# Performance work log

Measured on AMD Instinct MI355X. Metric: run time of the kernel, lower is better.

## Reference

```python
import jax, jax.numpy as jnp
import numpy as np

D_MODEL = 1024
H = 16
D_K = D_MODEL // H
B = 4
S = 2048
NEG = -1.0e9


def setup_inputs() -> dict:
    key = jax.random.key(0)
    ks = jax.random.split(key, 12)
    scale = 1.0 / np.sqrt(D_MODEL)
    inp = {
        "q": jax.random.normal(ks[0], (B, S, D_MODEL), jnp.float32),
        "k": jax.random.normal(ks[1], (B, S, D_MODEL), jnp.float32),
        "v": jax.random.normal(ks[2], (B, S, D_MODEL), jnp.float32),
        "mask": jax.random.randint(ks[3], (1, 1, S, S), 0, 2, jnp.int32),
        # nn.Linear params: y = x @ W.T + b
        "Wq": jax.random.normal(ks[4], (D_MODEL, D_MODEL), jnp.float32) * scale,
        "bq": jnp.zeros((D_MODEL,), jnp.float32),
        "Wk": jax.random.normal(ks[5], (D_MODEL, D_MODEL), jnp.float32) * scale,
        "bk": jnp.zeros((D_MODEL,), jnp.float32),
        "Wv": jax.random.normal(ks[6], (D_MODEL, D_MODEL), jnp.float32) * scale,
        "bv": jnp.zeros((D_MODEL,), jnp.float32),
        "Wo": jax.random.normal(ks[7], (D_MODEL, D_MODEL), jnp.float32) * scale,
        "bo": jnp.zeros((D_MODEL,), jnp.float32),
    }
    return inp


def reference(q, k, v, mask, Wq, bq, Wk, bk, Wv, bv, Wo, bo):
    # QKV projections (torch Linear: x @ W.T + b)
    query = q @ Wq.T + bq                       # [B,S,D]
    key_ = k @ Wk.T + bk
    value = v @ Wv.T + bv
    # [B,S,D] -> [B,H,S,d_k]
    def split_heads(x):
        return x.reshape(B, S, H, D_K).transpose(0, 2, 1, 3)
    query, key_, value = split_heads(query), split_heads(key_), split_heads(value)
    # scaled dot-product attention
    scores = jnp.einsum("bhqd,bhkd->bhqk", query, key_) / np.sqrt(D_K)
    scores = jnp.where(mask == 0, NEG, scores)  # masked_fill(mask==0, -1e9)
    attn = jax.nn.softmax(scores, axis=-1)      # dropout p=0 -> identity
    x = jnp.einsum("bhqk,bhkd->bhqd", attn, value)
    # merge heads and output projection
    x = x.transpose(0, 2, 1, 3).reshape(B, S, D_MODEL)
    return x @ Wo.T + bo
```

## Files before the change

### kernel.cpp

```cpp
#include <hip/hip_runtime.h>
#include <hip/hip_bf16.h>

typedef __bf16 bf16;
typedef __bf16 bf16x8 __attribute__((ext_vector_type(8)));
typedef __bf16 bf16x4 __attribute__((ext_vector_type(4)));
typedef float  f32x4v __attribute__((ext_vector_type(4)));

#define MFMA16(a, b, c) __builtin_amdgcn_mfma_f32_16x16x32_bf16((a), (b), (c), 0, 0, 0)

static constexpr int D_MODEL = 1024;
static constexpr int NH      = 16;
static constexpr int DK      = 64;
static constexpr int BATCH   = 4;
static constexpr int SEQ     = 2048;

__device__ __forceinline__ void glds16(const void* g, void* l) {
    __builtin_amdgcn_global_load_lds((const __attribute__((address_space(1))) void*)g,
                                     (__attribute__((address_space(3))) void*)l, 16, 0, 0);
}

struct CvtArgs {
    const float* s[7];
    bf16* d[7];
    int n[7];
};

__global__ __launch_bounds__(256) void cvt7(CvtArgs a) {
    const int which = blockIdx.y;
    const int i = (blockIdx.x * 256 + threadIdx.x) * 8;
    if (i >= a.n[which]) return;
    const float4 v0 = *(const float4*)(a.s[which] + i);
    const float4 v1 = *(const float4*)(a.s[which] + i + 4);
    bf16x8 o = {(bf16)v0.x, (bf16)v0.y, (bf16)v0.z, (bf16)v0.w,
                (bf16)v1.x, (bf16)v1.y, (bf16)v1.z, (bf16)v1.w};
    *(bf16x8*)(a.d[which] + i) = o;
}

__global__ __launch_bounds__(256) void mask_prep(const int* __restrict__ m,
                                                 bf16* __restrict__ Mr) {
    const int o = blockIdx.x * 256 + threadIdx.x;
    const int row = o >> 11, j = o & 2047;
    const int g = j >> 6, idx = j & 63;
    const int incol = (g << 6) + ((idx & 3) << 4) + (idx >> 2);
    Mr[o] = (bf16)(float)m[row * 2048 + incol];
}

template <int MODE>
__global__ __launch_bounds__(256) void gemm_bt(const bf16* __restrict__ A,
                                               const bf16* __restrict__ W,
                                               const float* __restrict__ bias,
                                               void* __restrict__ outv) {
    __shared__ bf16 Als[128 * 32];
    __shared__ bf16 Bls[128 * 32];

    const int tid  = threadIdx.x;
    const int wave = tid >> 6;
    const int lane = tid & 63;
    const int l15  = lane & 15;
    const int quad = lane >> 4;
    const int m0   = blockIdx.y * 128;
    const int n0   = blockIdx.x * 128;
    const int wm   = (wave >> 1) * 64;
    const int wn   = (wave & 1) * 64;

    f32x4v acc[4][4];
#pragma unroll
    for (int i = 0; i < 4; ++i)
#pragma unroll
        for (int j = 0; j < 4; ++j) acc[i][j] = (f32x4v){0.f, 0.f, 0.f, 0.f};

    const int r_a    = wave * 16 + (lane >> 2);
    const int c_a    = (lane & 3) * 8;
    const int ldsoff = wave * 512;

    for (int k0 = 0; k0 < 1024; k0 += 32) {
        __syncthreads();
#pragma unroll
        for (int p = 0; p < 2; ++p) {
            const int row = p * 64 + r_a;
            glds16(A + (size_t)(m0 + row) * 1024 + k0 + c_a, &Als[p * 2048 + ldsoff]);
            glds16(W + (size_t)(n0 + row) * 1024 + k0 + c_a, &Bls[p * 2048 + ldsoff]);
        }
        __syncthreads();

        bf16x8 af[4], bfr[4];
#pragma unroll
        for (int i = 0; i < 4; ++i)
            af[i] = *(const bf16x8*)(&Als[(wm + i * 16 + l15) * 32 + quad * 8]);
#pragma unroll
        for (int j = 0; j < 4; ++j)
            bfr[j] = *(const bf16x8*)(&Bls[(wn + j * 16 + l15) * 32 + quad * 8]);
#pragma unroll
        for (int i = 0; i < 4; ++i)
#pragma unroll
            for (int j = 0; j < 4; ++j) acc[i][j] = MFMA16(af[i], bfr[j], acc[i][j]);
    }

#pragma unroll
    for (int j = 0; j < 4; ++j) {
        const int col = n0 + wn + j * 16 + l15;
        const float bs = bias[col];
        const int h = col >> 6, dk = col & 63;
#pragma unroll
        for (int i = 0; i < 4; ++i) {
            const int r4 = m0 + wm + i * 16 + quad * 4;
            const int b = r4 >> 11, sb = r4 & 2047;
            if (MODE == 2) {
                float* out = (float*)outv;
#pragma unroll
                for (int reg = 0; reg < 4; ++reg)
                    out[(size_t)(r4 + reg) * 1024 + col] = acc[i][j][reg] + bs;
            } else if (MODE == 0) {
                bf16* out = (bf16*)outv;
#pragma unroll
                for (int reg = 0; reg < 4; ++reg)
                    out[((size_t)(b * NH + h) * SEQ + sb + reg) * 64 + dk] =
                        (bf16)(acc[i][j][reg] + bs);
            } else {
                bf16* out = (bf16*)outv;
                bf16x4 v = {(bf16)(acc[i][j][0] + bs), (bf16)(acc[i][j][1] + bs),
                            (bf16)(acc[i][j][2] + bs), (bf16)(acc[i][j][3] + bs)};
                *(bf16x4*)(&out[((size_t)((b * NH + h) * 64 + dk)) * SEQ + sb]) = v;
            }
        }
    }
}

__global__ __launch_bounds__(256) void attn_kernel(const bf16* __restrict__ Qh,
                                                   const bf16* __restrict__ Kh,
                                                   const bf16* __restrict__ Vtg,
                                                   const bf16* __restrict__ Mr,
                                                   bf16* __restrict__ Xout) {
    __shared__ bf16 Kls[4096];
    __shared__ bf16 Vls[4096];
    __shared__ bf16 Pls[256 * 72];

    const int tid  = threadIdx.x;
    const int wave = tid >> 6;
    const int lane = tid & 63;
    const int l15  = lane & 15;
    const int quad = lane >> 4;
    const int bh   = blockIdx.x;
    const int q0   = blockIdx.y * 256;

    const size_t base = (size_t)bh * SEQ * DK;
    const bf16* Q  = Qh + base;
    const bf16* K  = Kh + base;
    const bf16* Vg = Vtg + base;

    const int qw = q0 + wave * 64;
    bf16x8 aq[4][2];
#pragma unroll
    for (int rb = 0; rb < 4; ++rb)
#pragma unroll
        for (int hf = 0; hf < 2; ++hf)
            aq[rb][hf] = *(const bf16x8*)(Q + (size_t)(qw + rb * 16 + l15) * 64 +
                                          hf * 32 + quad * 8);

    f32x4v acc[4][4];
    float lsum[4][4];
#pragma unroll
    for (int rb = 0; rb < 4; ++rb)
#pragma unroll
        for (int x = 0; x < 4; ++x) {
            acc[rb][x] = (f32x4v){0.f, 0.f, 0.f, 0.f};
            lsum[rb][x] = 0.f;
        }

    constexpr float CLOG = 0.125f * 1.4426950408889634f;
    const bf16* mbase = Mr + (size_t)(qw + quad * 4) * 2048 + l15 * 4;

    for (int kt = 0; kt < SEQ; kt += 64) {
        __syncthreads();
#pragma unroll
        for (int p = 0; p < 2; ++p) {
            const int kc = wave * 2 + p;
            glds16(K + (size_t)(kt + lane) * 64 + kc * 8, &Kls[kc * 512]);
            glds16(Vg + (size_t)lane * SEQ + kt + kc * 8, &Vls[kc * 512]);
        }
        bf16x4 mv[4][4];
#pragma unroll
        for (int rb = 0; rb < 4; ++rb)
#pragma unroll
            for (int reg = 0; reg < 4; ++reg)
                mv[rb][reg] = *(const bf16x4*)(mbase + (size_t)(rb * 16 + reg) * 2048 + kt);
        __syncthreads();

        bf16x8 bk[4][2];
#pragma unroll
        for (int n16 = 0; n16 < 4; ++n16)
#pragma unroll
            for (int kk = 0; kk < 2; ++kk)
                bk[n16][kk] = *(const bf16x8*)(&Kls[((kk * 4 + quad) * 64 + n16 * 16 + l15) * 8]);

#pragma unroll
        for (int rb = 0; rb < 4; ++rb) {
            f32x4v sv[4];
#pragma unroll
            for (int n16 = 0; n16 < 4; ++n16) {
                f32x4v t = (f32x4v){0.f, 0.f, 0.f, 0.f};
                t = MFMA16(aq[rb][0], bk[n16][0], t);
                t = MFMA16(aq[rb][1], bk[n16][1], t);
                sv[n16] = t;
            }
            const int prow0 = wave * 64 + rb * 16 + quad * 4;
#pragma unroll
            for (int reg = 0; reg < 4; ++reg) {
#pragma unroll
                for (int n16 = 0; n16 < 4; ++n16) {
                    const float e =
                        exp2f(sv[n16][reg] * CLOG) * (float)mv[rb][reg][n16];
                    lsum[rb][reg] += e;
                    Pls[(prow0 + reg) * 72 + n16 * 16 + l15] = (bf16)e;
                }
            }
        }

        bf16x8 pf[4][2];
#pragma unroll
        for (int rb = 0; rb < 4; ++rb)
#pragma unroll
            for (int kc2 = 0; kc2 < 2; ++kc2)
                pf[rb][kc2] = *(const bf16x8*)(&Pls[(wave * 64 + rb * 16 + l15) * 72 +
                                                    kc2 * 32 + quad * 8]);
#pragma unroll
        for (int nt = 0; nt < 4; ++nt) {
            const bf16x8 bv0 = *(const bf16x8*)(&Vls[(quad * 64 + nt * 16 + l15) * 8]);
            const bf16x8 bv1 = *(const bf16x8*)(&Vls[((4 + quad) * 64 + nt * 16 + l15) * 8]);
#pragma unroll
            for (int rb = 0; rb < 4; ++rb) {
                acc[rb][nt] = MFMA16(pf[rb][0], bv0, acc[rb][nt]);
                acc[rb][nt] = MFMA16(pf[rb][1], bv1, acc[rb][nt]);
            }
        }
    }

    const int b = bh >> 4, h = bh & 15;
#pragma unroll
    for (int rb = 0; rb < 4; ++rb) {
        float rinv[4];
#pragma unroll
        for (int reg = 0; reg < 4; ++reg) {
            float l = lsum[rb][reg];
            l += __shfl_xor(l, 1, 16);
            l += __shfl_xor(l, 2, 16);
            l += __shfl_xor(l, 4, 16);
            l += __shfl_xor(l, 8, 16);
            rinv[reg] = 1.0f / l;
        }
#pragma unroll
        for (int nt = 0; nt < 4; ++nt)
#pragma unroll
            for (int reg = 0; reg < 4; ++reg) {
                const int sg = qw + rb * 16 + quad * 4 + reg;
                Xout[(size_t)(b * SEQ + sg) * D_MODEL + h * 64 + nt * 16 + l15] =
                    (bf16)(acc[rb][nt][reg] * rinv[reg]);
            }
    }
}

extern "C" void kernel_launch(void* const* d_in, const int* in_sizes, int n_in,
                              void* d_out, int out_size, void* d_ws, size_t ws_size,
                              hipStream_t stream) {
    const float* q    = (const float*)d_in[0];
    const float* k    = (const float*)d_in[1];
    const float* v    = (const float*)d_in[2];
    const int*   mask = (const int*)d_in[3];
    const float* Wq   = (const float*)d_in[4];
    const float* bq   = (const float*)d_in[5];
    const float* Wk   = (const float*)d_in[6];
    const float* bk   = (const float*)d_in[7];
    const float* Wv   = (const float*)d_in[8];
    const float* bv   = (const float*)d_in[9];
    const float* Wo   = (const float*)d_in[10];
    const float* bo   = (const float*)d_in[11];

    const size_t T = (size_t)BATCH * SEQ * D_MODEL;
    const size_t WN = (size_t)D_MODEL * D_MODEL;
    char* w = (char*)d_ws;
    bf16* Qh  = (bf16*)w;            w += T * 2;
    bf16* Kh  = (bf16*)w;            w += T * 2;
    bf16* Vt  = (bf16*)w;            w += T * 2;
    bf16* Mr  = (bf16*)w;            w += (size_t)SEQ * SEQ * 2;
    bf16* qb  = (bf16*)w;            w += T * 2;
    bf16* kb  = (bf16*)w;            w += T * 2;
    bf16* vb  = (bf16*)w;            w += T * 2;
    bf16* Wqb = (bf16*)w;            w += WN * 2;
    bf16* Wkb = (bf16*)w;            w += WN * 2;
    bf16* Wvb = (bf16*)w;            w += WN * 2;
    bf16* Wob = (bf16*)w;            w += WN * 2;

    CvtArgs ca;
    ca.s[0] = q;  ca.d[0] = qb;  ca.n[0] = (int)T;
    ca.s[1] = k;  ca.d[1] = kb;  ca.n[1] = (int)T;
    ca.s[2] = v;  ca.d[2] = vb;  ca.n[2] = (int)T;
    ca.s[3] = Wq; ca.d[3] = Wqb; ca.n[3] = (int)WN;
    ca.s[4] = Wk; ca.d[4] = Wkb; ca.n[4] = (int)WN;
    ca.s[5] = Wv; ca.d[5] = Wvb; ca.n[5] = (int)WN;
    ca.s[6] = Wo; ca.d[6] = Wob; ca.n[6] = (int)WN;

    cvt7<<<dim3(4096, 7), 256, 0, stream>>>(ca);
    mask_prep<<<dim3((SEQ * SEQ) / 256), 256, 0, stream>>>(mask, Mr);

    dim3 gg(D_MODEL / 128, (BATCH * SEQ) / 128);
    gemm_bt<0><<<gg, 256, 0, stream>>>(qb, Wqb, bq, (void*)Qh);
    gemm_bt<0><<<gg, 256, 0, stream>>>(kb, Wkb, bk, (void*)Kh);
    gemm_bt<1><<<gg, 256, 0, stream>>>(vb, Wvb, bv, (void*)Vt);

    attn_kernel<<<dim3(BATCH * NH, SEQ / 256), 256, 0, stream>>>(Qh, Kh, Vt, Mr, qb);

    gemm_bt<2><<<gg, 256, 0, stream>>>(qb, Wob, bo, d_out);
}
```

Measured before the change: 452.8 us.

## Batch QKV GEMMs, keep P in registers, shrink attention tile, vectorize preprocessing

Merges the three QKV projection launches into one z-batched launch and turns the conversion kernel into a grid-stride loop with fewer blocks. The mask prep now copies the mask without permuting it, reading and writing eight elements per thread. The attention kernel computes the transposed score tile (K as the A operand), so the softmax probabilities stay in registers as the B operand of the PV MFMA, with no LDS round trip for P. Each wave now handles 32 query rows instead of 64, doubling the grid, and output stores are vectorized. The intent is to cut LDS traffic, syncs and launch overhead, at the cost of more K/V tile reloads per query and per-lane V gathers assembled from two 4-wide LDS reads.

```diff
diff --git a/kernel.cpp b/kernel.cpp
--- a/kernel.cpp
+++ b/kernel.cpp
@@ -27,75 +27,81 @@
 
 __global__ __launch_bounds__(256) void cvt7(CvtArgs a) {
     const int which = blockIdx.y;
-    const int i = (blockIdx.x * 256 + threadIdx.x) * 8;
-    if (i >= a.n[which]) return;
-    const float4 v0 = *(const float4*)(a.s[which] + i);
-    const float4 v1 = *(const float4*)(a.s[which] + i + 4);
-    bf16x8 o = {(bf16)v0.x, (bf16)v0.y, (bf16)v0.z, (bf16)v0.w,
-                (bf16)v1.x, (bf16)v1.y, (bf16)v1.z, (bf16)v1.w};
-    *(bf16x8*)(a.d[which] + i) = o;
+    const int n = a.n[which];
+    const float* __restrict__ s = a.s[which];
+    bf16* __restrict__ d = a.d[which];
+    for (int i = (blockIdx.x * 256 + threadIdx.x) * 8; i < n; i += 512 * 256 * 8) {
+        const float4 v0 = *(const float4*)(s + i);
+        const float4 v1 = *(const float4*)(s + i + 4);
+        bf16x8 o = {(bf16)v0.x, (bf16)v0.y, (bf16)v0.z, (bf16)v0.w,
+                    (bf16)v1.x, (bf16)v1.y, (bf16)v1.z, (bf16)v1.w};
+        *(bf16x8*)(d + i) = o;
+    }
 }
 
 __global__ __launch_bounds__(256) void mask_prep(const int* __restrict__ m,
                                                  bf16* __restrict__ Mr) {
-    const int o = blockIdx.x * 256 + threadIdx.x;
-    const int row = o >> 11, j = o & 2047;
-    const int g = j >> 6, idx = j & 63;
-    const int incol = (g << 6) + ((idx & 3) << 4) + (idx >> 2);
-    Mr[o] = (bf16)(float)m[row * 2048 + incol];
-}
-
-template <int MODE>
-__global__ __launch_bounds__(256) void gemm_bt(const bf16* __restrict__ A,
-                                               const bf16* __restrict__ W,
-                                               const float* __restrict__ bias,
-                                               void* __restrict__ outv) {
-    __shared__ bf16 Als[128 * 32];
-    __shared__ bf16 Bls[128 * 32];
-
-    const int tid  = threadIdx.x;
-    const int wave = tid >> 6;
-    const int lane = tid & 63;
-    const int l15  = lane & 15;
-    const int quad = lane >> 4;
-    const int m0   = blockIdx.y * 128;
-    const int n0   = blockIdx.x * 128;
-    const int wm   = (wave >> 1) * 64;
-    const int wn   = (wave & 1) * 64;
-
-    f32x4v acc[4][4];
-#pragma unroll
-    for (int i = 0; i < 4; ++i)
-#pragma unroll
-        for (int j = 0; j < 4; ++j) acc[i][j] = (f32x4v){0.f, 0.f, 0.f, 0.f};
-
-    const int r_a    = wave * 16 + (lane >> 2);
-    const int c_a    = (lane & 3) * 8;
-    const int ldsoff = wave * 512;
-
-    for (int k0 = 0; k0 < 1024; k0 += 32) {
-        __syncthreads();
-#pragma unroll
-        for (int p = 0; p < 2; ++p) {
-            const int row = p * 64 + r_a;
-            glds16(A + (size_t)(m0 + row) * 1024 + k0 + c_a, &Als[p * 2048 + ldsoff]);
-            glds16(W + (size_t)(n0 + row) * 1024 + k0 + c_a, &Bls[p * 2048 + ldsoff]);
-        }
-        __syncthreads();
-
-        bf16x8 af[4], bfr[4];
-#pragma unroll
-        for (int i = 0; i < 4; ++i)
-            af[i] = *(const bf16x8*)(&Als[(wm + i * 16 + l15) * 32 + quad * 8]);
-#pragma unroll
-        for (int j = 0; j < 4; ++j)
-            bfr[j] = *(const bf16x8*)(&Bls[(wn + j * 16 + l15) * 32 + quad * 8]);
-#pragma unroll
-        for (int i = 0; i < 4; ++i)
-#pragma unroll
-            for (int j = 0; j < 4; ++j) acc[i][j] = MFMA16(af[i], bfr[j], acc[i][j]);
-    }
-
+    const int i = (blockIdx.x * 256 + threadIdx.x) * 8;
+    const int4 a = *(const int4*)(m + i);
+    const int4 b = *(const int4*)(m + i + 4);
+    bf16x8 o = {(bf16)(float)a.x, (bf16)(float)a.y, (bf16)(float)a.z, (bf16)(float)a.w,
+                (bf16)(float)b.x, (bf16)(float)b.y, (bf16)(float)b.z, (bf16)(float)b.w};
+    *(bf16x8*)(Mr + i) = o;
+}
+
+struct GemmBatch {
+    const bf16* A[3];
+    const bf16* W[3];
+    const float* bias[3];
+    bf16* out[3];
+};
+
+#define GEMM_KLOOP(Aptr, Wptr)                                                      \
+    __shared__ bf16 Als[128 * 32];                                                  \
+    __shared__ bf16 Bls[128 * 32];                                                  \
+    const int tid  = threadIdx.x;                                                   \
+    const int wave = tid >> 6;                                                      \
+    const int lane = tid & 63;                                                      \
+    const int l15  = lane & 15;                                                     \
+    const int quad = lane >> 4;                                                     \
+    const int m0   = blockIdx.y * 128;                                              \
+    const int n0   = blockIdx.x * 128;                                              \
+    const int wm   = (wave >> 1) * 64;                                              \
+    const int wn   = (wave & 1) * 64;                                               \
+    f32x4v acc[4][4];                                                               \
+    _Pragma("unroll") for (int i = 0; i < 4; ++i)                                   \
+        _Pragma("unroll") for (int j = 0; j < 4; ++j)                               \
+            acc[i][j] = (f32x4v){0.f, 0.f, 0.f, 0.f};                               \
+    const int r_a    = wave * 16 + (lane >> 2);                                     \
+    const int c_a    = (lane & 3) * 8;                                              \
+    const int ldsoff = wave * 512;                                                  \
+    for (int k0 = 0; k0 < 1024; k0 += 32) {                                         \
+        __syncthreads();                                                            \
+        _Pragma("unroll") for (int p = 0; p < 2; ++p) {                             \
+            const int row = p * 64 + r_a;                                           \
+            glds16(Aptr + (size_t)(m0 + row) * 1024 + k0 + c_a,                     \
+                   &Als[p * 2048 + ldsoff]);                                        \
+            glds16(Wptr + (size_t)(n0 + row) * 1024 + k0 + c_a,                     \
+                   &Bls[p * 2048 + ldsoff]);                                        \
+        }                                                                           \
+        __syncthreads();                                                            \
+        bf16x8 af[4], bfr[4];                                                       \
+        _Pragma("unroll") for (int i = 0; i < 4; ++i)                               \
+            af[i] = *(const bf16x8*)(&Als[(wm + i * 16 + l15) * 32 + quad * 8]);    \
+        _Pragma("unroll") for (int j = 0; j < 4; ++j)                               \
+            bfr[j] = *(const bf16x8*)(&Bls[(wn + j * 16 + l15) * 32 + quad * 8]);   \
+        _Pragma("unroll") for (int i = 0; i < 4; ++i)                               \
+            _Pragma("unroll") for (int j = 0; j < 4; ++j)                           \
+                acc[i][j] = MFMA16(af[i], bfr[j], acc[i][j]);                       \
+    }
+
+__global__ __launch_bounds__(256) void gemm_qkv(GemmBatch g) {
+    const int z = blockIdx.z;
+    const bf16* __restrict__ A = g.A[z];
+    const bf16* __restrict__ W = g.W[z];
+    GEMM_KLOOP(A, W)
+    const float* __restrict__ bias = g.bias[z];
+    bf16* __restrict__ out = g.out[z];
 #pragma unroll
     for (int j = 0; j < 4; ++j) {
         const int col = n0 + wn + j * 16 + l15;
@@ -105,23 +111,35 @@
         for (int i = 0; i < 4; ++i) {
             const int r4 = m0 + wm + i * 16 + quad * 4;
             const int b = r4 >> 11, sb = r4 & 2047;
-            if (MODE == 2) {
-                float* out = (float*)outv;
-#pragma unroll
-                for (int reg = 0; reg < 4; ++reg)
-                    out[(size_t)(r4 + reg) * 1024 + col] = acc[i][j][reg] + bs;
-            } else if (MODE == 0) {
-                bf16* out = (bf16*)outv;
+            if (z == 2) {
+                bf16x4 v = {(bf16)(acc[i][j][0] + bs), (bf16)(acc[i][j][1] + bs),
+                            (bf16)(acc[i][j][2] + bs), (bf16)(acc[i][j][3] + bs)};
+                *(bf16x4*)(&out[((size_t)((b * NH + h) * 64 + dk)) * SEQ + sb]) = v;
+            } else {
 #pragma unroll
                 for (int reg = 0; reg < 4; ++reg)
                     out[((size_t)(b * NH + h) * SEQ + sb + reg) * 64 + dk] =
                         (bf16)(acc[i][j][reg] + bs);
-            } else {
-                bf16* out = (bf16*)outv;
-                bf16x4 v = {(bf16)(acc[i][j][0] + bs), (bf16)(acc[i][j][1] + bs),
-                            (bf16)(acc[i][j][2] + bs), (bf16)(acc[i][j][3] + bs)};
-                *(bf16x4*)(&out[((size_t)((b * NH + h) * 64 + dk)) * SEQ + sb]) = v;
             }
+        }
+    }
+}
+
+__global__ __launch_bounds__(256) void gemm_o(const bf16* __restrict__ A,
+                                              const bf16* __restrict__ W,
+                                              const float* __restrict__ bias,
+                                              float* __restrict__ out) {
+    GEMM_KLOOP(A, W)
+#pragma unroll
+    for (int j = 0; j < 4; ++j) {
+        const int col = n0 + wn + j * 16 + l15;
+        const float bs = bias[col];
+#pragma unroll
+        for (int i = 0; i < 4; ++i) {
+            const int r4 = m0 + wm + i * 16 + quad * 4;
+#pragma unroll
+            for (int reg = 0; reg < 4; ++reg)
+                out[(size_t)(r4 + reg) * 1024 + col] = acc[i][j][reg] + bs;
         }
     }
 }
@@ -133,7 +151,6 @@
                                                    bf16* __restrict__ Xout) {
     __shared__ bf16 Kls[4096];
     __shared__ bf16 Vls[4096];
-    __shared__ bf16 Pls[256 * 72];
 
     const int tid  = threadIdx.x;
     const int wave = tid >> 6;
@@ -141,34 +158,31 @@
     const int l15  = lane & 15;
     const int quad = lane >> 4;
     const int bh   = blockIdx.x;
-    const int q0   = blockIdx.y * 256;
+    const int q0   = blockIdx.y * 128;
 
     const size_t base = (size_t)bh * SEQ * DK;
     const bf16* Q  = Qh + base;
     const bf16* K  = Kh + base;
     const bf16* Vg = Vtg + base;
 
-    const int qw = q0 + wave * 64;
-    bf16x8 aq[4][2];
-#pragma unroll
-    for (int rb = 0; rb < 4; ++rb)
-#pragma unroll
-        for (int hf = 0; hf < 2; ++hf)
-            aq[rb][hf] = *(const bf16x8*)(Q + (size_t)(qw + rb * 16 + l15) * 64 +
-                                          hf * 32 + quad * 8);
-
-    f32x4v acc[4][4];
-    float lsum[4][4];
-#pragma unroll
-    for (int rb = 0; rb < 4; ++rb)
-#pragma unroll
-        for (int x = 0; x < 4; ++x) {
-            acc[rb][x] = (f32x4v){0.f, 0.f, 0.f, 0.f};
-            lsum[rb][x] = 0.f;
-        }
+    const int qw = q0 + wave * 32;
+    bf16x8 aq[2][2];
+#pragma unroll
+    for (int qb = 0; qb < 2; ++qb)
+#pragma unroll
+        for (int kk = 0; kk < 2; ++kk)
+            aq[qb][kk] = *(const bf16x8*)(Q + (size_t)(qw + qb * 16 + l15) * 64 +
+                                          kk * 32 + quad * 8);
+
+    f32x4v acc[2][4];
+    float lsum[2] = {0.f, 0.f};
+#pragma unroll
+    for (int qb = 0; qb < 2; ++qb)
+#pragma unroll
+        for (int nt = 0; nt < 4; ++nt) acc[qb][nt] = (f32x4v){0.f, 0.f, 0.f, 0.f};
 
     constexpr float CLOG = 0.125f * 1.4426950408889634f;
-    const bf16* mbase = Mr + (size_t)(qw + quad * 4) * 2048 + l15 * 4;
+    const bf16* mrow = Mr + (size_t)(qw + l15) * 2048 + quad * 4;
 
     for (int kt = 0; kt < SEQ; kt += 64) {
         __syncthreads();
@@ -178,84 +192,80 @@
             glds16(K + (size_t)(kt + lane) * 64 + kc * 8, &Kls[kc * 512]);
             glds16(Vg + (size_t)lane * SEQ + kt + kc * 8, &Vls[kc * 512]);
         }
-        bf16x4 mv[4][4];
-#pragma unroll
-        for (int rb = 0; rb < 4; ++rb)
-#pragma unroll
-            for (int reg = 0; reg < 4; ++reg)
-                mv[rb][reg] = *(const bf16x4*)(mbase + (size_t)(rb * 16 + reg) * 2048 + kt);
+        bf16x4 mv[2][4];
+#pragma unroll
+        for (int qb = 0; qb < 2; ++qb)
+#pragma unroll
+            for (int t16 = 0; t16 < 4; ++t16)
+                mv[qb][t16] = *(const bf16x4*)(mrow + qb * 16 * 2048 + kt + t16 * 16);
         __syncthreads();
 
-        bf16x8 bk[4][2];
-#pragma unroll
-        for (int n16 = 0; n16 < 4; ++n16)
-#pragma unroll
-            for (int kk = 0; kk < 2; ++kk)
-                bk[n16][kk] = *(const bf16x8*)(&Kls[((kk * 4 + quad) * 64 + n16 * 16 + l15) * 8]);
-
-#pragma unroll
-        for (int rb = 0; rb < 4; ++rb) {
-            f32x4v sv[4];
-#pragma unroll
-            for (int n16 = 0; n16 < 4; ++n16) {
-                f32x4v t = (f32x4v){0.f, 0.f, 0.f, 0.f};
-                t = MFMA16(aq[rb][0], bk[n16][0], t);
-                t = MFMA16(aq[rb][1], bk[n16][1], t);
-                sv[n16] = t;
+        f32x4v sv[2][4];
+#pragma unroll
+        for (int qb = 0; qb < 2; ++qb)
+#pragma unroll
+            for (int t16 = 0; t16 < 4; ++t16) sv[qb][t16] = (f32x4v){0.f, 0.f, 0.f, 0.f};
+#pragma unroll
+        for (int kk = 0; kk < 2; ++kk) {
+#pragma unroll
+            for (int t16 = 0; t16 < 4; ++t16) {
+                const bf16x8 bk =
+                    *(const bf16x8*)(&Kls[((kk * 4 + quad) * 64 + t16 * 16 + l15) * 8]);
+                sv[0][t16] = MFMA16(bk, aq[0][kk], sv[0][t16]);
+                sv[1][t16] = MFMA16(bk, aq[1][kk], sv[1][t16]);
             }
-            const int prow0 = wave * 64 + rb * 16 + quad * 4;
-#pragma unroll
-            for (int reg = 0; reg < 4; ++reg) {
-#pragma unroll
-                for (int n16 = 0; n16 < 4; ++n16) {
-                    const float e =
-                        exp2f(sv[n16][reg] * CLOG) * (float)mv[rb][reg][n16];
-                    lsum[rb][reg] += e;
-                    Pls[(prow0 + reg) * 72 + n16 * 16 + l15] = (bf16)e;
+        }
+
+        bf16x8 pf[2][2];
+#pragma unroll
+        for (int qb = 0; qb < 2; ++qb) {
+#pragma unroll
+            for (int h = 0; h < 2; ++h) {
+#pragma unroll
+                for (int t16h = 0; t16h < 2; ++t16h) {
+                    const int t16 = 2 * h + t16h;
+#pragma unroll
+                    for (int r = 0; r < 4; ++r) {
+                        const float e = exp2f(sv[qb][t16][r] * CLOG) *
+                                        (float)mv[qb][t16][r];
+                        lsum[qb] += e;
+                        pf[qb][h][t16h * 4 + r] = (bf16)e;
+                    }
                 }
             }
         }
 
-        bf16x8 pf[4][2];
-#pragma unroll
-        for (int rb = 0; rb < 4; ++rb)
-#pragma unroll
-            for (int kc2 = 0; kc2 < 2; ++kc2)
-                pf[rb][kc2] = *(const bf16x8*)(&Pls[(wave * 64 + rb * 16 + l15) * 72 +
-                                                    kc2 * 32 + quad * 8]);
 #pragma unroll
         for (int nt = 0; nt < 4; ++nt) {
-            const bf16x8 bv0 = *(const bf16x8*)(&Vls[(quad * 64 + nt * 16 + l15) * 8]);
-            const bf16x8 bv1 = *(const bf16x8*)(&Vls[((4 + quad) * 64 + nt * 16 + l15) * 8]);
-#pragma unroll
-            for (int rb = 0; rb < 4; ++rb) {
-                acc[rb][nt] = MFMA16(pf[rb][0], bv0, acc[rb][nt]);
-                acc[rb][nt] = MFMA16(pf[rb][1], bv1, acc[rb][nt]);
+            const int d = nt * 16 + l15;
+#pragma unroll
+            for (int h = 0; h < 2; ++h) {
+                const bf16x4 v0 = *(const bf16x4*)(
+                    &Vls[((4 * h + (quad >> 1)) * 64 + d) * 8 + (quad & 1) * 4]);
+                const bf16x4 v1 = *(const bf16x4*)(
+                    &Vls[((4 * h + 2 + (quad >> 1)) * 64 + d) * 8 + (quad & 1) * 4]);
+                const bf16x8 va = {v0[0], v0[1], v0[2], v0[3],
+                                   v1[0], v1[1], v1[2], v1[3]};
+                acc[0][nt] = MFMA16(va, pf[0][h], acc[0][nt]);
+                acc[1][nt] = MFMA16(va, pf[1][h], acc[1][nt]);
             }
         }
     }
 
     const int b = bh >> 4, h = bh & 15;
 #pragma unroll
-    for (int rb = 0; rb < 4; ++rb) {
-        float rinv[4];
-#pragma unroll
-        for (int reg = 0; reg < 4; ++reg) {
-            float l = lsum[rb][reg];
-            l += __shfl_xor(l, 1, 16);
-            l += __shfl_xor(l, 2, 16);
-            l += __shfl_xor(l, 4, 16);
-            l += __shfl_xor(l, 8, 16);
-            rinv[reg] = 1.0f / l;
-        }
-#pragma unroll
-        for (int nt = 0; nt < 4; ++nt)
-#pragma unroll
-            for (int reg = 0; reg < 4; ++reg) {
-                const int sg = qw + rb * 16 + quad * 4 + reg;
-                Xout[(size_t)(b * SEQ + sg) * D_MODEL + h * 64 + nt * 16 + l15] =
-                    (bf16)(acc[rb][nt][reg] * rinv[reg]);
-            }
+    for (int qb = 0; qb < 2; ++qb) {
+        float l = lsum[qb];
+        l += __shfl_xor(l, 16, 64);
+        l += __shfl_xor(l, 32, 64);
+        const float rinv = 1.0f / l;
+        const size_t rowoff = (size_t)(b * SEQ + qw + qb * 16 + l15) * D_MODEL;
+#pragma unroll
+        for (int nt = 0; nt < 4; ++nt) {
+            bf16x4 o = {(bf16)(acc[qb][nt][0] * rinv), (bf16)(acc[qb][nt][1] * rinv),
+                        (bf16)(acc[qb][nt][2] * rinv), (bf16)(acc[qb][nt][3] * rinv)};
+            *(bf16x4*)(&Xout[rowoff + h * 64 + nt * 16 + quad * 4]) = o;
+        }
     }
 }
 
@@ -278,36 +288,37 @@
     const size_t T = (size_t)BATCH * SEQ * D_MODEL;
     const size_t WN = (size_t)D_MODEL * D_MODEL;
     char* w = (char*)d_ws;
-    bf16* Qh  = (bf16*)w;            w += T * 2;
-    bf16* Kh  = (bf16*)w;            w += T * 2;
-    bf16* Vt  = (bf16*)w;            w += T * 2;
-    bf16* Mr  = (bf16*)w;            w += (size_t)SEQ * SEQ * 2;
-    bf16* qb  = (bf16*)w;            w += T * 2;
-    bf16* kb  = (bf16*)w;            w += T * 2;
-    bf16* vb  = (bf16*)w;            w += T * 2;
-    bf16* Wqb = (bf16*)w;            w += WN * 2;
-    bf16* Wkb = (bf16*)w;            w += WN * 2;
-    bf16* Wvb = (bf16*)w;            w += WN * 2;
-    bf16* Wob = (bf16*)w;            w += WN * 2;
+    bf16* Qh  = (bf16*)w; w += T * 2;
+    bf16* Kh  = (bf16*)w; w += T * 2;
+    bf16* Vt  = (bf16*)w; w += T * 2;
+    bf16* Mr  = (bf16*)w; w += (size_t)SEQ * SEQ * 2;
+    bf16* qb2 = (bf16*)w; w += T * 2;
+    bf16* kb2 = (bf16*)w; w += T * 2;
+    bf16* vb2 = (bf16*)w; w += T * 2;
+    bf16* Wqb = (bf16*)w; w += WN * 2;
+    bf16* Wkb = (bf16*)w; w += WN * 2;
+    bf16* Wvb = (bf16*)w; w += WN * 2;
+    bf16* Wob = (bf16*)w; w += WN * 2;
 
     CvtArgs ca;
-    ca.s[0] = q;  ca.d[0] = qb;  ca.n[0] = (int)T;
-    ca.s[1] = k;  ca.d[1] = kb;  ca.n[1] = (int)T;
-    ca.s[2] = v;  ca.d[2] = vb;  ca.n[2] = (int)T;
+    ca.s[0] = q;  ca.d[0] = qb2; ca.n[0] = (int)T;
+    ca.s[1] = k;  ca.d[1] = kb2; ca.n[1] = (int)T;
+    ca.s[2] = v;  ca.d[2] = vb2; ca.n[2] = (int)T;
     ca.s[3] = Wq; ca.d[3] = Wqb; ca.n[3] = (int)WN;
     ca.s[4] = Wk; ca.d[4] = Wkb; ca.n[4] = (int)WN;
     ca.s[5] = Wv; ca.d[5] = Wvb; ca.n[5] = (int)WN;
     ca.s[6] = Wo; ca.d[6] = Wob; ca.n[6] = (int)WN;
-
-    cvt7<<<dim3(4096, 7), 256, 0, stream>>>(ca);
-    mask_prep<<<dim3((SEQ * SEQ) / 256), 256, 0, stream>>>(mask, Mr);
-
-    dim3 gg(D_MODEL / 128, (BATCH * SEQ) / 128);
-    gemm_bt<0><<<gg, 256, 0, stream>>>(qb, Wqb, bq, (void*)Qh);
-    gemm_bt<0><<<gg, 256, 0, stream>>>(kb, Wkb, bk, (void*)Kh);
-    gemm_bt<1><<<gg, 256, 0, stream>>>(vb, Wvb, bv, (void*)Vt);
-
-    attn_kernel<<<dim3(BATCH * NH, SEQ / 256), 256, 0, stream>>>(Qh, Kh, Vt, Mr, qb);
-
-    gemm_bt<2><<<gg, 256, 0, stream>>>(qb, Wob, bo, d_out);
-}
+    cvt7<<<dim3(512, 7), 256, 0, stream>>>(ca);
+    mask_prep<<<dim3((SEQ * SEQ) / 2048), 256, 0, stream>>>(mask, Mr);
+
+    GemmBatch g;
+    g.A[0] = qb2; g.W[0] = Wqb; g.bias[0] = bq; g.out[0] = Qh;
+    g.A[1] = kb2; g.W[1] = Wkb; g.bias[1] = bk; g.out[1] = Kh;
+    g.A[2] = vb2; g.W[2] = Wvb; g.bias[2] = bv; g.out[2] = Vt;
+    gemm_qkv<<<dim3(D_MODEL / 128, (BATCH * SEQ) / 128, 3), 256, 0, stream>>>(g);
+
+    attn_kernel<<<dim3(BATCH * NH, SEQ / 128), 256, 0, stream>>>(Qh, Kh, Vt, Mr, qb2);
+
+    gemm_o<<<dim3(D_MODEL / 128, (BATCH * SEQ) / 128), 256, 0, stream>>>(qb2, Wob, bo,
+                                                                         (float*)d_out);
+}
```

Result: slower. 511.2 us (+12.9%).
